# Kernel optimization log

Measured on AMD Instinct MI355X. Metric: run time of the kernel, lower is better.

## Reference

```python
import jax, jax.numpy as jnp
import numpy as np

B, M, H, D = 2, 16384, 8, 64
HID = H * D
SEG = 128          # segment_lengths[0]
DIL = 2            # dilation_rates[0]


def _hilbert_perm(m):
    """perm[d] = row-major token index of the d-th point on the Hilbert curve
    over an n x n grid (n = sqrt(m), power of 2). Vectorized d2xy."""
    n = int(round(np.sqrt(m)))
    assert n * n == m and (n & (n - 1)) == 0
    t = np.arange(m, dtype=np.int64)
    x = np.zeros(m, np.int64)
    y = np.zeros(m, np.int64)
    s = 1
    while s < n:
        rx = 1 & (t // 2)
        ry = 1 & (t ^ rx)
        swap = ry == 0
        flip = swap & (rx == 1)
        xf = np.where(flip, s - 1 - x, x)
        yf = np.where(flip, s - 1 - y, y)
        x, y = np.where(swap, yf, xf), np.where(swap, xf, yf)
        x = x + s * rx
        y = y + s * ry
        t = t // 4
        s *= 2
    return y * n + x


_PERM = _hilbert_perm(M)
_INV = np.empty(M, np.int64)
_INV[_PERM] = np.arange(M)
PERM = jnp.asarray(_PERM)
INV_PERM = jnp.asarray(_INV)


def setup_inputs() -> dict:
    key = jax.random.key(0)
    ks = jax.random.split(key, 8)
    sc = 0.02
    return {
        "q": jax.random.normal(ks[0], (B, M, H, D), jnp.float32),
        "k": jax.random.normal(ks[1], (B, M, H, D), jnp.float32),
        "v": jax.random.normal(ks[2], (B, M, H, D), jnp.float32),
        # wrapper projections (nn.Linear without bias; stored [in, out])
        "Wq": jax.random.normal(ks[3], (HID, HID), jnp.float32) * sc,
        "Wk": jax.random.normal(ks[4], (HID, HID), jnp.float32) * sc,
        "Wv": jax.random.normal(ks[5], (HID, HID), jnp.float32) * sc,
        # HilbertAttentionCore fused qkv projection
        "Wqkv": jax.random.normal(ks[6], (HID, 3 * HID), jnp.float32) * sc,
        # wrapper output projection
        "Wout": jax.random.normal(ks[7], (HID, HID), jnp.float32) * sc,
    }


def _hilbert_attention(x, Wqkv):
    """x: [B, M, HID] -> [B, M, HID]. Hilbert reorder + segmented dilated attn."""
    b, m, _ = x.shape
    qkv = x @ Wqkv                                    # [B, M, 3*HID]
    qkv = qkv.reshape(b, m, 3, H, D)
    # Hilbert-curve reordering of the sequence (gather)
    qkv = qkv[:, PERM]                                # [B, M, 3, H, D]
    nseg = m // SEG
    g = SEG // DIL                                    # tokens per dilated group
    # [B, nseg, g, DIL, 3, H, D]: group r holds positions r, r+DIL, ... in seg
    qkv = qkv.reshape(b, nseg, g, DIL, 3, H, D)
    qh, kh, vh = qkv[..., 0, :, :], qkv[..., 1, :, :], qkv[..., 2, :, :]
    scale = 1.0 / jnp.sqrt(jnp.asarray(D, x.dtype))
    # attention within each (segment, dilation-group): t,s index the g tokens
    scores = jnp.einsum("bntrhd,bnsrhd->bnrhts", qh, kh) * scale
    attn = jax.nn.softmax(scores, axis=-1)
    out = jnp.einsum("bnrhts,bnsrhd->bntrhd", attn, vh)
    out = out.reshape(b, m, H, D)
    # inverse Hilbert reordering (scatter back)
    out = out[:, INV_PERM]
    return out.reshape(b, m, HID)


def reference(q, k, v, Wq, Wk, Wv, Wqkv, Wout):
    b, m, h, d = q.shape
    q_flat = q.reshape(b, m, h * d)
    k_flat = k.reshape(b, m, h * d)
    v_flat = v.reshape(b, m, h * d)
    x = (q_flat @ Wq + k_flat @ Wk + v_flat @ Wv) / 3.0
    out = _hilbert_attention(x, Wqkv)
    out = out @ Wout
    return out.reshape(b, m, h, d)
```

## Files before the change

### kernel.cpp

```cpp
#include <hip/hip_runtime.h>
#include <hip/hip_bf16.h>
#include <stdint.h>


typedef __bf16 bf16_t;
typedef __bf16 bf16x8 __attribute__((ext_vector_type(8)));
typedef float  f32x4  __attribute__((ext_vector_type(4)));

#define DEVI __device__ __forceinline__
#define SFENCE __builtin_amdgcn_sched_barrier(0)

static constexpr int Mtok = 16384;
static constexpr int ROWS = 32768;

DEVI void gload_lds16(const void* g, void* l) {
  __builtin_amdgcn_global_load_lds(
      (__attribute__((address_space(1))) uint32_t*)(uintptr_t)g,
      (__attribute__((address_space(3))) uint32_t*)(uint32_t)(uintptr_t)l,
      16, 0, 0);
}

__global__ void k_perm(int* __restrict__ perm) {
  int d = blockIdx.x * 256 + threadIdx.x;
  if (d >= Mtok) return;
  int t = d, x = 0, y = 0;
  for (int s = 1; s < 128; s <<= 1) {
    int rx = (t >> 1) & 1;
    int ry = (t ^ rx) & 1;
    if (ry == 0) {
      if (rx == 1) { x = s - 1 - x; y = s - 1 - y; }
      int tmp = x; x = y; y = tmp;
    }
    x += s * rx;
    y += s * ry;
    t >>= 2;
  }
  perm[d] = y * 128 + x;
}

__global__ void k_prep_w(const float* __restrict__ Wq, const float* __restrict__ Wk,
                         const float* __restrict__ Wv, const float* __restrict__ Wqkv,
                         const float* __restrict__ Wout,
                         bf16_t* __restrict__ W1t, bf16_t* __restrict__ Wqkvt,
                         bf16_t* __restrict__ Woutt) {
  const int tid = blockIdx.x * 256 + threadIdx.x;
  const int stride = gridDim.x * 256;
  for (int i = tid; i < 512 * 1536; i += stride) {
    int n = i / 1536, kk = i % 1536;
    const float* W = (kk < 512) ? Wq : (kk < 1024 ? Wk : Wv);
    W1t[i] = (bf16_t)(W[(kk & 511) * 512 + n] * (1.0f / 3.0f));
  }
  for (int i = tid; i < 1536 * 512; i += stride) {
    int n = i / 512, kk = i % 512;
    Wqkvt[i] = (bf16_t)Wqkv[kk * 1536 + n];
  }
  for (int i = tid; i < 512 * 512; i += stride) {
    int n = i / 512, kk = i % 512;
    Woutt[i] = (bf16_t)Wout[kk * 512 + n];
  }
}

DEVI void stageB(const bf16_t* Bb, int Kdim, int k0, bf16_t* dst, int qsel,
                 int tid, int cswz) {
  int r = tid >> 3;
  int rb0 = (r >> 5) * 64 + qsel * 32 + (r & 31);
  const bf16_t* g = Bb + (long)rb0 * Kdim + k0 + cswz * 8;
  gload_lds16(g, dst + rb0 * 64 + (tid & 7) * 8);
  gload_lds16(g + (long)128 * Kdim, dst + (rb0 + 128) * 64 + (tid & 7) * 8);
}

DEVI void stageA(const bf16_t* Ab, int Kdim, int k0, bf16_t* dst, int qsel,
                 int tid, int cswz) {
  int r = tid >> 3;
  int row0 = r + qsel * 64;
  const bf16_t* g = Ab + (long)row0 * Kdim + k0 + cswz * 8;
  gload_lds16(g, dst + row0 * 64 + (tid & 7) * 8);
  gload_lds16(g + (long)128 * Kdim, dst + (row0 + 128) * 64 + (tid & 7) * 8);
}

#define PHASE(QM, QN, STAGE_STMT, TAIL_STMT)                                   \
  do {                                                                         \
    bf16x8 af[4][2], bg[2][2];                                                 \
    _Pragma("unroll") for (int m = 0; m < 4; m++) {                            \
      int row = wm * 128 + (QM) * 64 + m * 16 + l15;                           \
      af[m][0] = *(const bf16x8*)(Acur + row * 64 + cb0 * 8);                  \
      af[m][1] = *(const bf16x8*)(Acur + row * 64 + cb1 * 8);                  \
    }                                                                          \
    _Pragma("unroll") for (int n = 0; n < 2; n++) {                            \
      int row = wn * 64 + (QN) * 32 + n * 16 + l15;                            \
      bg[n][0] = *(const bf16x8*)(Bcur + row * 64 + cb0 * 8);                  \
      bg[n][1] = *(const bf16x8*)(Bcur + row * 64 + cb1 * 8);                  \
    }                                                                          \
    STAGE_STMT;                                                                \
    SFENCE; __builtin_amdgcn_s_barrier(); SFENCE;                              \
    __builtin_amdgcn_s_setprio(1);                                             \
    _Pragma("unroll") for (int m = 0; m < 4; m++)                              \
    _Pragma("unroll") for (int n = 0; n < 2; n++) {                            \
      acc[(QM)*4+m][(QN)*2+n] = __builtin_amdgcn_mfma_f32_16x16x32_bf16(       \
          af[m][0], bg[n][0], acc[(QM)*4+m][(QN)*2+n], 0, 0, 0);               \
      acc[(QM)*4+m][(QN)*2+n] = __builtin_amdgcn_mfma_f32_16x16x32_bf16(       \
          af[m][1], bg[n][1], acc[(QM)*4+m][(QN)*2+n], 0, 0, 0);               \
    }                                                                          \
    __builtin_amdgcn_s_setprio(0);                                             \
    TAIL_STMT;                                                                 \
    SFENCE; __builtin_amdgcn_s_barrier(); SFENCE;                              \
  } while (0)

template <bool OUTF32>
__global__ __launch_bounds__(512, 2) void k_gemm256(const bf16_t* __restrict__ A,
                                                    const bf16_t* __restrict__ Bt,
                                                    bf16_t* __restrict__ Cb,
                                                    float* __restrict__ Cf,
                                                    int Ndim, int Kdim) {
  __shared__ bf16_t lds[4 * 16384];
  const int tid = threadIdx.x;
  const int lane = tid & 63, w = tid >> 6;
  const int wm = w >> 2, wn = w & 3;
  const int l15 = lane & 15, l4 = lane >> 4;
  const int cb0 = l4 ^ (l15 & 7), cb1 = cb0 ^ 4;
  const int cswz = (tid & 7) ^ ((tid >> 3) & 7);
  const long arow0 = (long)blockIdx.y * 256;
  const long bcol0 = (long)blockIdx.x * 256;
  const bf16_t* Ab = A + arow0 * Kdim;
  const bf16_t* Bb = Bt + bcol0 * Kdim;
  const int NT = Kdim >> 6;

  bf16_t* Acur = lds;
  bf16_t* Bcur = lds + 16384;
  bf16_t* Anxt = lds + 32768;
  bf16_t* Bnxt = lds + 49152;

  f32x4 acc[8][4] = {};

  stageA(Ab, Kdim, 0, Acur, 0, tid, cswz);
  stageB(Bb, Kdim, 0, Bcur, 0, tid, cswz);
  stageA(Ab, Kdim, 0, Acur, 1, tid, cswz);
  stageB(Bb, Kdim, 0, Bcur, 1, tid, cswz);
  stageA(Ab, Kdim, 64, Anxt, 0, tid, cswz);
  stageB(Bb, Kdim, 64, Bnxt, 0, tid, cswz);
  asm volatile("s_waitcnt vmcnt(4)" ::: "memory");
  __builtin_amdgcn_s_barrier();
  SFENCE;

  for (int t = 0; t < NT; t++) {
    PHASE(0, 0, if (t + 1 < NT) stageA(Ab, Kdim, (t + 1) * 64, Anxt, 1, tid, cswz), );
    PHASE(0, 1, if (t + 1 < NT) stageB(Bb, Kdim, (t + 1) * 64, Bnxt, 1, tid, cswz), );
    PHASE(1, 0, if (t + 2 < NT) stageA(Ab, Kdim, (t + 2) * 64, Acur, 0, tid, cswz), );
    PHASE(1, 1, if (t + 2 < NT) stageB(Bb, Kdim, (t + 2) * 64, Bcur, 0, tid, cswz),
          if (t + 2 < NT) { asm volatile("s_waitcnt vmcnt(4)" ::: "memory"); }
          else            { asm volatile("s_waitcnt vmcnt(0)" ::: "memory"); });
    bf16_t* tA = Acur; Acur = Anxt; Anxt = tA;
    bf16_t* tB = Bcur; Bcur = Bnxt; Bnxt = tB;
  }

#pragma unroll
  for (int i = 0; i < 8; i++) {
#pragma unroll
    for (int j = 0; j < 4; j++) {
      long row = arow0 + wm * 128 + i * 16 + l4 * 4;
      long col = bcol0 + wn * 64 + j * 16 + l15;
#pragma unroll
      for (int r = 0; r < 4; r++) {
        if constexpr (OUTF32) Cf[(row + r) * Ndim + col] = acc[i][j][r];
        else                  Cb[(row + r) * Ndim + col] = (bf16_t)acc[i][j][r];
      }
    }
  }
}

DEVI const float* selsrc(int tt, const float* q, const float* k, const float* v) {
  return tt < 8 ? q : (tt < 16 ? k : v);
}

DEVI void loadAh(const float* S, long grow, int colf, float4* pa) {
  const float* p0 = S + grow * 512 + colf;
  pa[0] = *(const float4*)(p0);
  pa[1] = *(const float4*)(p0 + 4);
  const float* p1 = p0 + 128 * 512;
  pa[2] = *(const float4*)(p1);
  pa[3] = *(const float4*)(p1 + 4);
}

DEVI void writeAh(bf16_t* dst, int rbase, int cbt, const float4* pa) {
  bf16x8 o0, o1;
  o0[0] = (bf16_t)pa[0].x; o0[1] = (bf16_t)pa[0].y; o0[2] = (bf16_t)pa[0].z; o0[3] = (bf16_t)pa[0].w;
  o0[4] = (bf16_t)pa[1].x; o0[5] = (bf16_t)pa[1].y; o0[6] = (bf16_t)pa[1].z; o0[7] = (bf16_t)pa[1].w;
  o1[0] = (bf16_t)pa[2].x; o1[1] = (bf16_t)pa[2].y; o1[2] = (bf16_t)pa[2].z; o1[3] = (bf16_t)pa[2].w;
  o1[4] = (bf16_t)pa[3].x; o1[5] = (bf16_t)pa[3].y; o1[6] = (bf16_t)pa[3].z; o1[7] = (bf16_t)pa[3].w;
  int sw = (cbt ^ (rbase & 7)) * 8;
  *(bf16x8*)(dst + rbase * 64 + sw) = o0;
  *(bf16x8*)(dst + (rbase + 128) * 64 + sw) = o1;
}

#define PHASEF(QM, QN, S1, S2, S3, TAIL_STMT)                                  \
  do {                                                                         \
    bf16x8 af[4][2], bg[2][2];                                                 \
    _Pragma("unroll") for (int m = 0; m < 4; m++) {                            \
      int row = wm * 128 + (QM) * 64 + m * 16 + l15;                           \
      af[m][0] = *(const bf16x8*)(Acur + row * 64 + cb0 * 8);                  \
      af[m][1] = *(const bf16x8*)(Acur + row * 64 + cb1 * 8);                  \
    }                                                                          \
    _Pragma("unroll") for (int n = 0; n < 2; n++) {                            \
      int row = wn * 64 + (QN) * 32 + n * 16 + l15;                            \
      bg[n][0] = *(const bf16x8*)(Bcur + row * 64 + cb0 * 8);                  \
      bg[n][1] = *(const bf16x8*)(Bcur + row * 64 + cb1 * 8);                  \
    }                                                                          \
    S1;                                                                        \
    SFENCE;                                                                    \
    S2;                                                                        \
    SFENCE;                                                                    \
    S3;                                                                        \
    SFENCE; __builtin_amdgcn_s_barrier(); SFENCE;                              \
    __builtin_amdgcn_s_setprio(1);                                             \
    _Pragma("unroll") for (int m = 0; m < 4; m++)                              \
    _Pragma("unroll") for (int n = 0; n < 2; n++) {                            \
      acc[(QM)*4+m][(QN)*2+n] = __builtin_amdgcn_mfma_f32_16x16x32_bf16(       \
          af[m][0], bg[n][0], acc[(QM)*4+m][(QN)*2+n], 0, 0, 0);               \
      acc[(QM)*4+m][(QN)*2+n] = __builtin_amdgcn_mfma_f32_16x16x32_bf16(       \
          af[m][1], bg[n][1], acc[(QM)*4+m][(QN)*2+n], 0, 0, 0);               \
    }                                                                          \
    __builtin_amdgcn_s_setprio(0);                                             \
    TAIL_STMT;                                                                 \
    SFENCE; __builtin_amdgcn_s_barrier(); SFENCE;                              \
  } while (0)

__global__ __launch_bounds__(512, 2) void k_gemm1f(const float* __restrict__ q,
                                                   const float* __restrict__ k,
                                                   const float* __restrict__ v,
                                                   const bf16_t* __restrict__ Bt,
                                                   bf16_t* __restrict__ Cb,
                                                   int Ndim) {
  constexpr int Kdim = 1536;
  constexpr int NT = 24;
  __shared__ bf16_t lds[4 * 16384];
  const int tid = threadIdx.x;
  const int lane = tid & 63, w = tid >> 6;
  const int wm = w >> 2, wn = w & 3;
  const int l15 = lane & 15, l4 = lane >> 4;
  const int cb0 = l4 ^ (l15 & 7), cb1 = cb0 ^ 4;
  const int cswz = (tid & 7) ^ ((tid >> 3) & 7);
  const int cbt = tid & 7, rA = tid >> 3;
  const long arow0 = (long)blockIdx.y * 256;
  const long bcol0 = (long)blockIdx.x * 256;
  const bf16_t* Bb = Bt + bcol0 * Kdim;

  bf16_t* Acur = lds;
  bf16_t* Bcur = lds + 16384;
  bf16_t* Anxt = lds + 32768;
  bf16_t* Bnxt = lds + 49152;

  f32x4 acc[8][4] = {};
  float4 pa0[4], pa1[4];

  loadAh(selsrc(0, q, k, v), arow0 + rA,      (cbt << 3), pa0);
  loadAh(selsrc(0, q, k, v), arow0 + rA + 64, (cbt << 3), pa1);
  SFENCE;
  writeAh(Acur, rA,      cbt, pa0);
  writeAh(Acur, rA + 64, cbt, pa1);
  SFENCE;
  stageB(Bb, Kdim, 0, Bcur, 0, tid, cswz);
  stageB(Bb, Kdim, 0, Bcur, 1, tid, cswz);
  SFENCE;
  loadAh(selsrc(1, q, k, v), arow0 + rA,      64 + (cbt << 3), pa0);
  loadAh(selsrc(1, q, k, v), arow0 + rA + 64, 64 + (cbt << 3), pa1);
  SFENCE;
  stageB(Bb, Kdim, 64, Bnxt, 0, tid, cswz);
  SFENCE;
  asm volatile("s_waitcnt vmcnt(10)" ::: "memory");
  asm volatile("s_waitcnt lgkmcnt(0)" ::: "memory");
  __builtin_amdgcn_s_barrier();
  SFENCE;

  for (int t = 0; t < NT; t++) {
    PHASEF(0, 0,
           if (t + 1 < NT) writeAh(Anxt, rA, cbt, pa0),
           if (t + 2 < NT) loadAh(selsrc(t + 2, q, k, v), arow0 + rA,
                                  (((t + 2) & 7) << 6) + (cbt << 3), pa0),
           , );
    PHASEF(0, 1,
           if (t + 1 < NT) stageB(Bb, Kdim, (t + 1) * 64, Bnxt, 1, tid, cswz),
           if (t + 1 < NT) writeAh(Anxt, rA + 64, cbt, pa1),
           if (t + 2 < NT) loadAh(selsrc(t + 2, q, k, v), arow0 + rA + 64,
                                  (((t + 2) & 7) << 6) + (cbt << 3), pa1),
           );
    PHASEF(1, 0, , , , );
    PHASEF(1, 1,
           if (t + 2 < NT) stageB(Bb, Kdim, (t + 2) * 64, Bcur, 0, tid, cswz),
           , ,
           if (t + 2 < NT) { asm volatile("s_waitcnt vmcnt(6)" ::: "memory"); }
           else            { asm volatile("s_waitcnt vmcnt(0)" ::: "memory"); });
    bf16_t* tA = Acur; Acur = Anxt; Anxt = tA;
    bf16_t* tB = Bcur; Bcur = Bnxt; Bnxt = tB;
  }

#pragma unroll
  for (int i = 0; i < 8; i++) {
#pragma unroll
    for (int j = 0; j < 4; j++) {
      long row = arow0 + wm * 128 + i * 16 + l4 * 4;
      long col = bcol0 + wn * 64 + j * 16 + l15;
#pragma unroll
      for (int r = 0; r < 4; r++)
        Cb[(row + r) * Ndim + col] = (bf16_t)acc[i][j][r];
    }
  }
}

__global__ __launch_bounds__(256, 2) void k_attn(const bf16_t* __restrict__ QKV,
                                                 const int* __restrict__ perm,
                                                 bf16_t* __restrict__ ATT) {
  __shared__ bf16_t Vt[2][64 * 64];
  __shared__ bf16_t P[2][64 * 64];
  __shared__ bf16_t O[128 * 64];
  __shared__ int perml[128];
  const int n = blockIdx.x, h = blockIdx.y, b = blockIdx.z;
  const int t = threadIdx.x;
  const int lane = t & 63, w = t >> 6;
  const int l15 = lane & 15, l4 = lane >> 4;

  if (t < 128) perml[t] = perm[n * 128 + t];
  __syncthreads();

#pragma unroll
  for (int it = 0; it < 4; it++) {
    int c = t + it * 256;
    int tok = c >> 3, c8 = c & 7;
    long j = (long)b * Mtok + perml[tok];
    bf16x8 vv = *(const bf16x8*)(QKV + j * 1536 + 1024 + h * 64 + c8 * 8);
    int grp = tok & 1, s = tok >> 1;
    bf16_t* vt = Vt[grp];
#pragma unroll
    for (int i = 0; i < 8; i++) {
      int d = c8 * 8 + i;
      vt[d * 64 + (s ^ ((d & 7) << 3))] = vv[i];
    }
  }

  const int grp = w >> 1, th = w & 1;

  f32x4 sc[2][4] = {};
#pragma unroll
  for (int ks = 0; ks < 2; ks++) {
    bf16x8 aq[2], bk[4];
#pragma unroll
    for (int tf = 0; tf < 2; tf++) {
      int tq = th * 32 + tf * 16 + l15;
      long j = (long)b * Mtok + perml[tq * 2 + grp];
      aq[tf] = *(const bf16x8*)(QKV + j * 1536 + h * 64 + ks * 32 + l4 * 8);
    }
#pragma unroll
    for (int sf = 0; sf < 4; sf++) {
      int s = sf * 16 + l15;
      long j = (long)b * Mtok + perml[s * 2 + grp];
      bk[sf] = *(const bf16x8*)(QKV + j * 1536 + 512 + h * 64 + ks * 32 + l4 * 8);
    }
#pragma unroll
    for (int tf = 0; tf < 2; tf++)
#pragma unroll
      for (int sf = 0; sf < 4; sf++)
        sc[tf][sf] = __builtin_amdgcn_mfma_f32_16x16x32_bf16(aq[tf], bk[sf], sc[tf][sf], 0, 0, 0);
  }

  const float scale = 0.125f;
#pragma unroll
  for (int tf = 0; tf < 2; tf++) {
#pragma unroll
    for (int r = 0; r < 4; r++) {
      float mx = fmaxf(fmaxf(sc[tf][0][r], sc[tf][1][r]), fmaxf(sc[tf][2][r], sc[tf][3][r]));
      mx = fmaxf(mx, __shfl_xor(mx, 1, 64));
      mx = fmaxf(mx, __shfl_xor(mx, 2, 64));
      mx = fmaxf(mx, __shfl_xor(mx, 4, 64));
      mx = fmaxf(mx, __shfl_xor(mx, 8, 64));
      float p0 = __expf((sc[tf][0][r] - mx) * scale);
      float p1 = __expf((sc[tf][1][r] - mx) * scale);
      float p2 = __expf((sc[tf][2][r] - mx) * scale);
      float p3 = __expf((sc[tf][3][r] - mx) * scale);
      float sum = p0 + p1 + p2 + p3;
      sum += __shfl_xor(sum, 1, 64);
      sum += __shfl_xor(sum, 2, 64);
      sum += __shfl_xor(sum, 4, 64);
      sum += __shfl_xor(sum, 8, 64);
      float inv = 1.0f / sum;
      int trow = th * 32 + tf * 16 + l4 * 4 + r;
      int sw = (trow & 7) << 3;
      bf16_t* pp = P[grp];
      pp[trow * 64 + ((l15     ) ^ sw)] = (bf16_t)(p0 * inv);
      pp[trow * 64 + ((l15 + 16) ^ sw)] = (bf16_t)(p1 * inv);
      pp[trow * 64 + ((l15 + 32) ^ sw)] = (bf16_t)(p2 * inv);
      pp[trow * 64 + ((l15 + 48) ^ sw)] = (bf16_t)(p3 * inv);
    }
  }
  __syncthreads();

  f32x4 oacc[2][4] = {};
#pragma unroll
  for (int ks = 0; ks < 2; ks++) {
    bf16x8 ap[2], bv[4];
#pragma unroll
    for (int tf = 0; tf < 2; tf++) {
      int trow = th * 32 + tf * 16 + l15;
      int cb = (ks * 4 + l4) ^ (trow & 7);
      ap[tf] = *(const bf16x8*)(P[grp] + trow * 64 + cb * 8);
    }
#pragma unroll
    for (int df = 0; df < 4; df++) {
      int d = df * 16 + l15;
      int cb = (ks * 4 + l4) ^ (d & 7);
      bv[df] = *(const bf16x8*)(Vt[grp] + d * 64 + cb * 8);
    }
#pragma unroll
    for (int tf = 0; tf < 2; tf++)
#pragma unroll
      for (int df = 0; df < 4; df++)
        oacc[tf][df] = __builtin_amdgcn_mfma_f32_16x16x32_bf16(ap[tf], bv[df], oacc[tf][df], 0, 0, 0);
  }

#pragma unroll
  for (int tf = 0; tf < 2; tf++)
#pragma unroll
    for (int df = 0; df < 4; df++)
#pragma unroll
      for (int r = 0; r < 4; r++) {
        int trow = th * 32 + tf * 16 + l4 * 4 + r;
        int tok = trow * 2 + grp;
        O[tok * 64 + df * 16 + l15] = (bf16_t)oacc[tf][df][r];
      }
  __syncthreads();
#pragma unroll
  for (int it = 0; it < 4; it++) {
    int c = t + it * 256;
    int tok = c >> 3, c8 = c & 7;
    long j = (long)b * Mtok + perml[tok];
    *(bf16x8*)(ATT + j * 512 + h * 64 + c8 * 8) = *(const bf16x8*)(O + tok * 64 + c8 * 8);
  }
}

extern "C" void kernel_launch(void* const* d_in, const int* in_sizes, int n_in,
                              void* d_out, int out_size, void* d_ws, size_t ws_size,
                              hipStream_t stream) {
  const float* q    = (const float*)d_in[0];
  const float* k    = (const float*)d_in[1];
  const float* v    = (const float*)d_in[2];
  const float* Wq   = (const float*)d_in[3];
  const float* Wk   = (const float*)d_in[4];
  const float* Wv   = (const float*)d_in[5];
  const float* Wqkv = (const float*)d_in[6];
  const float* Wout = (const float*)d_in[7];

  char* ws = (char*)d_ws;
  const size_t QKV_BYTES = (size_t)ROWS * 1536 * 2;
  const size_t X_BYTES   = (size_t)ROWS * 512 * 2;
  bf16_t* QKV   = (bf16_t*)ws;
  bf16_t* X     = (bf16_t*)(ws + QKV_BYTES);
  bf16_t* W1t   = (bf16_t*)(ws + QKV_BYTES + X_BYTES);
  bf16_t* Wqkvt = W1t + 512 * 1536;
  bf16_t* Woutt = Wqkvt + 1536 * 512;
  int*    perm  = (int*)(Woutt + 512 * 512);

  k_perm<<<64, 256, 0, stream>>>(perm);
  k_prep_w<<<512, 256, 0, stream>>>(Wq, Wk, Wv, Wqkv, Wout, W1t, Wqkvt, Woutt);
  k_gemm1f<<<dim3(2, 128), 512, 0, stream>>>(q, k, v, W1t, X, 512);
  k_gemm256<false><<<dim3(6, 128), 512, 0, stream>>>(X, Wqkvt, QKV, nullptr, 1536, 512);
  k_attn<<<dim3(128, 8, 2), 256, 0, stream>>>(QKV, perm, X);
  k_gemm256<true><<<dim3(2, 128), 512, 0, stream>>>(X, Woutt, nullptr, (float*)d_out, 512, 512);
}
```

Baseline: 233.9 us.

## Reorder GEMM quadrant phases to reuse A/B fragments across quadrants

Restructures the 4-phase K-loop in both GEMM kernels so quadrants run in a serpentine order (00,01,11,10). A or B register fragments are kept across adjacent phases, which halves the LDS fragment reads per phase. The staging schedule shifts to match: A and B half-tiles are issued in new slots, and the fp32-input GEMM prefetches A one tile further ahead with deeper vmcnt waits. This adds register pressure from the extra fragment buffers and makes the wait counts and buffer reuse more fragile.

After: 229.2 us. 2.0% less time.

```diff
diff --git a/kernel.cpp b/kernel.cpp
--- a/kernel.cpp
+++ b/kernel.cpp
@@ -9,6 +9,7 @@
 
 #define DEVI __device__ __forceinline__
 #define SFENCE __builtin_amdgcn_sched_barrier(0)
+#define PH_BAR do { SFENCE; __builtin_amdgcn_s_barrier(); SFENCE; } while (0)
 
 static constexpr int Mtok = 16384;
 static constexpr int ROWS = 32768;
@@ -78,32 +79,27 @@
   gload_lds16(g + (long)128 * Kdim, dst + (row0 + 128) * 64 + (tid & 7) * 8);
 }
 
-#define PHASE(QM, QN, STAGE_STMT, TAIL_STMT)                                   \
+#define LOAD_AF(AF, QM, BUF)                                                   \
+  _Pragma("unroll") for (int m = 0; m < 4; m++) {                              \
+    int row = wm * 128 + (QM) * 64 + m * 16 + l15;                             \
+    AF[m][0] = *(const bf16x8*)((BUF) + row * 64 + cb0 * 8);                   \
+    AF[m][1] = *(const bf16x8*)((BUF) + row * 64 + cb1 * 8);                   \
+  }
+#define LOAD_BG(BG, QN, BUF)                                                   \
+  _Pragma("unroll") for (int n = 0; n < 2; n++) {                              \
+    int row = wn * 64 + (QN) * 32 + n * 16 + l15;                              \
+    BG[n][0] = *(const bf16x8*)((BUF) + row * 64 + cb0 * 8);                   \
+    BG[n][1] = *(const bf16x8*)((BUF) + row * 64 + cb1 * 8);                   \
+  }
+#define QUAD(QM, QN, AF, BG)                                                   \
   do {                                                                         \
-    bf16x8 af[4][2], bg[2][2];                                                 \
-    _Pragma("unroll") for (int m = 0; m < 4; m++) {                            \
-      int row = wm * 128 + (QM) * 64 + m * 16 + l15;                           \
-      af[m][0] = *(const bf16x8*)(Acur + row * 64 + cb0 * 8);                  \
-      af[m][1] = *(const bf16x8*)(Acur + row * 64 + cb1 * 8);                  \
-    }                                                                          \
-    _Pragma("unroll") for (int n = 0; n < 2; n++) {                            \
-      int row = wn * 64 + (QN) * 32 + n * 16 + l15;                            \
-      bg[n][0] = *(const bf16x8*)(Bcur + row * 64 + cb0 * 8);                  \
-      bg[n][1] = *(const bf16x8*)(Bcur + row * 64 + cb1 * 8);                  \
-    }                                                                          \
-    STAGE_STMT;                                                                \
-    SFENCE; __builtin_amdgcn_s_barrier(); SFENCE;                              \
     __builtin_amdgcn_s_setprio(1);                                             \
+    _Pragma("unroll") for (int kh = 0; kh < 2; kh++)                           \
     _Pragma("unroll") for (int m = 0; m < 4; m++)                              \
-    _Pragma("unroll") for (int n = 0; n < 2; n++) {                            \
+    _Pragma("unroll") for (int n = 0; n < 2; n++)                              \
       acc[(QM)*4+m][(QN)*2+n] = __builtin_amdgcn_mfma_f32_16x16x32_bf16(       \
-          af[m][0], bg[n][0], acc[(QM)*4+m][(QN)*2+n], 0, 0, 0);               \
-      acc[(QM)*4+m][(QN)*2+n] = __builtin_amdgcn_mfma_f32_16x16x32_bf16(       \
-          af[m][1], bg[n][1], acc[(QM)*4+m][(QN)*2+n], 0, 0, 0);               \
-    }                                                                          \
+          AF[m][kh], BG[n][kh], acc[(QM)*4+m][(QN)*2+n], 0, 0, 0);             \
     __builtin_amdgcn_s_setprio(0);                                             \
-    TAIL_STMT;                                                                 \
-    SFENCE; __builtin_amdgcn_s_barrier(); SFENCE;                              \
   } while (0)
 
 template <bool OUTF32>
@@ -133,22 +129,40 @@
   f32x4 acc[8][4] = {};
 
   stageA(Ab, Kdim, 0, Acur, 0, tid, cswz);
+  stageA(Ab, Kdim, 0, Acur, 1, tid, cswz);
   stageB(Bb, Kdim, 0, Bcur, 0, tid, cswz);
-  stageA(Ab, Kdim, 0, Acur, 1, tid, cswz);
   stageB(Bb, Kdim, 0, Bcur, 1, tid, cswz);
   stageA(Ab, Kdim, 64, Anxt, 0, tid, cswz);
-  stageB(Bb, Kdim, 64, Bnxt, 0, tid, cswz);
+  stageB(Bb, Kdim, 64, Bnxt, 1, tid, cswz);
   asm volatile("s_waitcnt vmcnt(4)" ::: "memory");
   __builtin_amdgcn_s_barrier();
   SFENCE;
 
   for (int t = 0; t < NT; t++) {
-    PHASE(0, 0, if (t + 1 < NT) stageA(Ab, Kdim, (t + 1) * 64, Anxt, 1, tid, cswz), );
-    PHASE(0, 1, if (t + 1 < NT) stageB(Bb, Kdim, (t + 1) * 64, Bnxt, 1, tid, cswz), );
-    PHASE(1, 0, if (t + 2 < NT) stageA(Ab, Kdim, (t + 2) * 64, Acur, 0, tid, cswz), );
-    PHASE(1, 1, if (t + 2 < NT) stageB(Bb, Kdim, (t + 2) * 64, Bcur, 0, tid, cswz),
-          if (t + 2 < NT) { asm volatile("s_waitcnt vmcnt(4)" ::: "memory"); }
-          else            { asm volatile("s_waitcnt vmcnt(0)" ::: "memory"); });
+    bf16x8 af[4][2], bg0[2][2], bg1[2][2];
+    LOAD_AF(af, 0, Acur);
+    LOAD_BG(bg0, 0, Bcur);
+    if (t + 1 < NT) stageB(Bb, Kdim, (t + 1) * 64, Bnxt, 0, tid, cswz);
+    PH_BAR;
+    QUAD(0, 0, af, bg0);
+    PH_BAR;
+    LOAD_BG(bg1, 1, Bcur);
+    if (t + 1 < NT) stageA(Ab, Kdim, (t + 1) * 64, Anxt, 1, tid, cswz);
+    PH_BAR;
+    QUAD(0, 1, af, bg1);
+    PH_BAR;
+    LOAD_AF(af, 1, Acur);
+    if (t + 2 < NT) stageA(Ab, Kdim, (t + 2) * 64, Acur, 0, tid, cswz);
+    PH_BAR;
+    QUAD(1, 1, af, bg1);
+    PH_BAR;
+    LOAD_BG(bg0, 0, Bcur);
+    if (t + 2 < NT) stageB(Bb, Kdim, (t + 2) * 64, Bcur, 1, tid, cswz);
+    PH_BAR;
+    QUAD(1, 0, af, bg0);
+    if (t + 2 < NT) { asm volatile("s_waitcnt vmcnt(4)" ::: "memory"); }
+    else            { asm volatile("s_waitcnt vmcnt(0)" ::: "memory"); }
+    PH_BAR;
     bf16_t* tA = Acur; Acur = Anxt; Anxt = tA;
     bf16_t* tB = Bcur; Bcur = Bnxt; Bnxt = tB;
   }
@@ -191,38 +205,6 @@
   *(bf16x8*)(dst + rbase * 64 + sw) = o0;
   *(bf16x8*)(dst + (rbase + 128) * 64 + sw) = o1;
 }
-
-#define PHASEF(QM, QN, S1, S2, S3, TAIL_STMT)                                  \
-  do {                                                                         \
-    bf16x8 af[4][2], bg[2][2];                                                 \
-    _Pragma("unroll") for (int m = 0; m < 4; m++) {                            \
-      int row = wm * 128 + (QM) * 64 + m * 16 + l15;                           \
-      af[m][0] = *(const bf16x8*)(Acur + row * 64 + cb0 * 8);                  \
-      af[m][1] = *(const bf16x8*)(Acur + row * 64 + cb1 * 8);                  \
-    }                                                                          \
-    _Pragma("unroll") for (int n = 0; n < 2; n++) {                            \
-      int row = wn * 64 + (QN) * 32 + n * 16 + l15;                            \
-      bg[n][0] = *(const bf16x8*)(Bcur + row * 64 + cb0 * 8);                  \
-      bg[n][1] = *(const bf16x8*)(Bcur + row * 64 + cb1 * 8);                  \
-    }                                                                          \
-    S1;                                                                        \
-    SFENCE;                                                                    \
-    S2;                                                                        \
-    SFENCE;                                                                    \
-    S3;                                                                        \
-    SFENCE; __builtin_amdgcn_s_barrier(); SFENCE;                              \
-    __builtin_amdgcn_s_setprio(1);                                             \
-    _Pragma("unroll") for (int m = 0; m < 4; m++)                              \
-    _Pragma("unroll") for (int n = 0; n < 2; n++) {                            \
-      acc[(QM)*4+m][(QN)*2+n] = __builtin_amdgcn_mfma_f32_16x16x32_bf16(       \
-          af[m][0], bg[n][0], acc[(QM)*4+m][(QN)*2+n], 0, 0, 0);               \
-      acc[(QM)*4+m][(QN)*2+n] = __builtin_amdgcn_mfma_f32_16x16x32_bf16(       \
-          af[m][1], bg[n][1], acc[(QM)*4+m][(QN)*2+n], 0, 0, 0);               \
-    }                                                                          \
-    __builtin_amdgcn_s_setprio(0);                                             \
-    TAIL_STMT;                                                                 \
-    SFENCE; __builtin_amdgcn_s_barrier(); SFENCE;                              \
-  } while (0)
 
 __global__ __launch_bounds__(512, 2) void k_gemm1f(const float* __restrict__ q,
                                                    const float* __restrict__ k,
@@ -261,34 +243,53 @@
   stageB(Bb, Kdim, 0, Bcur, 0, tid, cswz);
   stageB(Bb, Kdim, 0, Bcur, 1, tid, cswz);
   SFENCE;
-  loadAh(selsrc(1, q, k, v), arow0 + rA,      64 + (cbt << 3), pa0);
-  loadAh(selsrc(1, q, k, v), arow0 + rA + 64, 64 + (cbt << 3), pa1);
-  SFENCE;
-  stageB(Bb, Kdim, 64, Bnxt, 0, tid, cswz);
-  SFENCE;
-  asm volatile("s_waitcnt vmcnt(10)" ::: "memory");
+  loadAh(selsrc(1, q, k, v), arow0 + rA, 64 + (cbt << 3), pa0);
+  SFENCE;
+  writeAh(Anxt, rA, cbt, pa0);
+  SFENCE;
+  stageB(Bb, Kdim, 64, Bnxt, 1, tid, cswz);
+  SFENCE;
+  loadAh(selsrc(1, q, k, v), arow0 + rA + 64,  64 + (cbt << 3), pa1);
+  loadAh(selsrc(2, q, k, v), arow0 + rA,      128 + (cbt << 3), pa0);
+  SFENCE;
+  asm volatile("s_waitcnt vmcnt(18)" ::: "memory");
   asm volatile("s_waitcnt lgkmcnt(0)" ::: "memory");
   __builtin_amdgcn_s_barrier();
   SFENCE;
 
   for (int t = 0; t < NT; t++) {
-    PHASEF(0, 0,
-           if (t + 1 < NT) writeAh(Anxt, rA, cbt, pa0),
-           if (t + 2 < NT) loadAh(selsrc(t + 2, q, k, v), arow0 + rA,
-                                  (((t + 2) & 7) << 6) + (cbt << 3), pa0),
-           , );
-    PHASEF(0, 1,
-           if (t + 1 < NT) stageB(Bb, Kdim, (t + 1) * 64, Bnxt, 1, tid, cswz),
-           if (t + 1 < NT) writeAh(Anxt, rA + 64, cbt, pa1),
-           if (t + 2 < NT) loadAh(selsrc(t + 2, q, k, v), arow0 + rA + 64,
-                                  (((t + 2) & 7) << 6) + (cbt << 3), pa1),
-           );
-    PHASEF(1, 0, , , , );
-    PHASEF(1, 1,
-           if (t + 2 < NT) stageB(Bb, Kdim, (t + 2) * 64, Bcur, 0, tid, cswz),
-           , ,
-           if (t + 2 < NT) { asm volatile("s_waitcnt vmcnt(6)" ::: "memory"); }
-           else            { asm volatile("s_waitcnt vmcnt(0)" ::: "memory"); });
+    bf16x8 af[4][2], bg0[2][2], bg1[2][2];
+    LOAD_AF(af, 0, Acur);
+    LOAD_BG(bg0, 0, Bcur);
+    if (t + 1 < NT) stageB(Bb, Kdim, (t + 1) * 64, Bnxt, 0, tid, cswz);
+    PH_BAR;
+    QUAD(0, 0, af, bg0);
+    PH_BAR;
+    LOAD_BG(bg1, 1, Bcur);
+    if (t + 1 < NT) writeAh(Anxt, rA + 64, cbt, pa1);
+    SFENCE;
+    if (t + 2 < NT) loadAh(selsrc(t + 2, q, k, v), arow0 + rA + 64,
+                           (((t + 2) & 7) << 6) + (cbt << 3), pa1);
+    PH_BAR;
+    QUAD(0, 1, af, bg1);
+    PH_BAR;
+    LOAD_AF(af, 1, Acur);
+    if (t + 2 < NT) writeAh(Acur, rA, cbt, pa0);
+    SFENCE;
+    if (t + 3 < NT) loadAh(selsrc(t + 3, q, k, v), arow0 + rA,
+                           (((t + 3) & 7) << 6) + (cbt << 3), pa0);
+    PH_BAR;
+    QUAD(1, 1, af, bg1);
+    PH_BAR;
+    LOAD_BG(bg0, 0, Bcur);
+    if (t + 2 < NT) stageB(Bb, Kdim, (t + 2) * 64, Bcur, 1, tid, cswz);
+    PH_BAR;
+    QUAD(1, 0, af, bg0);
+    if (t + 3 < NT)      { asm volatile("s_waitcnt vmcnt(18)" ::: "memory"); }
+    else if (t + 2 < NT) { asm volatile("s_waitcnt vmcnt(10)" ::: "memory"); }
+    else                 { asm volatile("s_waitcnt vmcnt(0)"  ::: "memory"); }
+    asm volatile("s_waitcnt lgkmcnt(0)" ::: "memory");
+    PH_BAR;
     bf16_t* tA = Acur; Acur = Anxt; Anxt = tA;
     bf16_t* tB = Bcur; Bcur = Bnxt; Bnxt = tB;
   }
```
